# Kernel tuning notes

Measured on AMD Instinct MI355X. Metric: run time of the kernel, lower is better.

## Reference

```python
import jax, jax.numpy as jnp
import numpy as np

NQ = 4       # num_qubits
DEPTH = 2
NC = 4       # num_classes
DIM = 2 ** NQ
EPS = 1e-5   # BatchNorm1d eps


def _cz_diag():
    # diagonal of the CZ chain on wires (0,1),(1,2),(2,3); wire w -> bit (NQ-1-w)
    d = np.ones(DIM, np.float32)
    for i in range(NQ - 1):
        for k in range(DIM):
            if ((k >> (NQ - 1 - i)) & 1) and ((k >> (NQ - 2 - i)) & 1):
                d[k] *= -1.0
    return jnp.asarray(d.astype(np.complex64))


def _zmat():
    # ZMAT[k, w] = <k|Z_w|k>
    z = np.empty((DIM, NQ), np.float32)
    for k in range(DIM):
        for w in range(NQ):
            z[k, w] = 1.0 - 2.0 * ((k >> (NQ - 1 - w)) & 1)
    return jnp.asarray(z)


CZ_DIAG = _cz_diag()
ZMAT = _zmat()


def _apply_1q(state, gate, wire):
    # state: [B, DIM] complex64; gate: [2,2] (shared) or [B,2,2] (batched)
    B = state.shape[0]
    left, right = 2 ** wire, 2 ** (NQ - 1 - wire)
    s = state.reshape(B, left, 2, right)
    if gate.ndim == 2:
        s = jnp.einsum('ij,bljr->blir', gate, s)
    else:
        s = jnp.einsum('bij,bljr->blir', gate, s)
    return s.reshape(B, DIM)


def _circuit(pooled, weights):
    # pooled: [B, NQ] angles; weights: [DEPTH*NQ]
    B = pooled.shape[0]
    state = jnp.zeros((B, DIM), jnp.complex64).at[:, 0].set(1.0)
    # RX(pooled[:, i]) on wire i  (batched gates)
    for i in range(NQ):
        th = pooled[:, i] * 0.5
        c, s = jnp.cos(th), jnp.sin(th)
        g = jnp.stack([jnp.stack([c, -1j * s], -1),
                       jnp.stack([-1j * s, c], -1)], -2)  # [B,2,2] complex64
        state = _apply_1q(state, g, i)
    idx = 0
    for _ in range(DEPTH):
        # RY(weights[idx]) on each wire (real 2x2, shared across batch)
        for i in range(NQ):
            th = weights[idx] * 0.5
            idx += 1
            c, s = jnp.cos(th), jnp.sin(th)
            g = jnp.stack([jnp.stack([c, -s]), jnp.stack([s, c])])  # [2,2]
            state = _apply_1q(state, g, i)
        # CZ chain = diagonal sign flips
        state = state * CZ_DIAG
    probs = state.real ** 2 + state.imag ** 2          # [B, DIM]
    return probs @ ZMAT                                # [B, NQ] expvals of Z_w


def setup_inputs() -> dict:
    B = 262144
    keys = jax.random.split(jax.random.key(0), 4)
    x = jax.random.normal(keys[0], (B, 1, 12, 12), jnp.float32)
    weights = jax.random.normal(keys[1], (DEPTH * NQ,), jnp.float32)
    W = jax.random.normal(keys[2], (NC, NQ), jnp.float32) * 0.5
    b = jax.random.normal(keys[3], (NC,), jnp.float32) * 0.1
    gamma = jnp.ones((NC,), jnp.float32)
    beta = jnp.zeros((NC,), jnp.float32)
    return {'x': x, 'weights': weights, 'W': W, 'b': b,
            'gamma': gamma, 'beta': beta}


def reference(x, weights, W, b, gamma, beta):
    B = x.shape[0]
    # avg_pool2d(x, 6): [B,1,12,12] -> [B,1,2,2] -> [B,4]
    pooled = x.reshape(B, 1, 2, 6, 2, 6).mean(axis=(3, 5)).reshape(B, NQ)
    q = _circuit(pooled, weights)                      # [B, NQ]
    logits = q @ W.T + b                               # [B, NC]
    # BatchNorm1d, training mode: batch mean / biased variance
    mean = logits.mean(axis=0)
    var = logits.var(axis=0)
    return (logits - mean) / jnp.sqrt(var + EPS) * gamma + beta
```

## Files before the change

kernel.cpp:

```cpp
#include <hip/hip_runtime.h>
#include <hip/hip_bf16.h>


__device__ __forceinline__ float bfbits2f(unsigned short u) {
    return __uint_as_float(((unsigned int)u) << 16);
}
__device__ __forceinline__ float ldp(const void* p, int i, bool isbf16) {
    if (isbf16) return bfbits2f(((const unsigned short*)p)[i]);
    return ((const float*)p)[i];
}
__device__ __forceinline__ int quad_of(int e) {
    return ((e / 12) / 6) * 2 + ((e % 12) / 6);
}

__global__ __launch_bounds__(256) void qcircuit_kernel(
    const void* __restrict__ x,
    const void* __restrict__ wts,
    const void* __restrict__ Wm,
    const void* __restrict__ bias,
    const void* __restrict__ gamma,
    float* __restrict__ logits,
    float* __restrict__ partials,
    int B)
{
    const int b = blockIdx.x * blockDim.x + threadIdx.x;
    if (b >= B) return;

    const bool isbf16 = (*(const unsigned int*)gamma) == 0x3F803F80u;

    float sums[4] = {0.f, 0.f, 0.f, 0.f};
    if (isbf16) {
        const uint4* px = reinterpret_cast<const uint4*>(x) + (size_t)b * 18;
        uint4 v[18];
#pragma unroll
        for (int i = 0; i < 18; ++i) v[i] = px[i];
#pragma unroll
        for (int i = 0; i < 18; ++i) {
            unsigned int wrd[4] = {v[i].x, v[i].y, v[i].z, v[i].w};
#pragma unroll
            for (int c = 0; c < 4; ++c) {
                const int e0 = i * 8 + c * 2;
                sums[quad_of(e0)]     += __uint_as_float(wrd[c] << 16);
                sums[quad_of(e0 + 1)] += __uint_as_float(wrd[c] & 0xffff0000u);
            }
        }
    } else {
        const float4* px = reinterpret_cast<const float4*>(x) + (size_t)b * 36;
#pragma unroll
        for (int i = 0; i < 36; ++i) {
            float4 t = px[i];
            const int e0 = i * 4;
            sums[quad_of(e0)]     += t.x;
            sums[quad_of(e0 + 1)] += t.y;
            sums[quad_of(e0 + 2)] += t.z;
            sums[quad_of(e0 + 3)] += t.w;
        }
    }

    const float pscale = 0.5f / 36.0f;
    float cg[4], sg[4];
#pragma unroll
    for (int w = 0; w < 4; ++w) {
        float th = sums[w] * pscale;
        sincosf(th, &sg[w], &cg[w]);
    }

    float f[16];
#pragma unroll
    for (int k = 0; k < 16; ++k) {
        float a0 = (k & 8) ? sg[0] : cg[0];
        float a1 = (k & 4) ? sg[1] : cg[1];
        float a2 = (k & 2) ? sg[2] : cg[2];
        float a3 = (k & 1) ? sg[3] : cg[3];
        f[k] = (a0 * a1) * (a2 * a3);
    }
    float re[16], im[16];
#pragma unroll
    for (int k = 0; k < 16; ++k) {
        int pc = __popc(k) & 3;
        re[k] = (pc == 0) ? f[k] : ((pc == 2) ? -f[k] : 0.f);
        im[k] = (pc == 3) ? f[k] : ((pc == 1) ? -f[k] : 0.f);
    }

    float wc[8], wsn[8];
#pragma unroll
    for (int i = 0; i < 8; ++i) {
        float th = ldp(wts, i, isbf16) * 0.5f;
        sincosf(th, &wsn[i], &wc[i]);
    }

#pragma unroll
    for (int d = 0; d < 2; ++d) {
#pragma unroll
        for (int w = 0; w < 4; ++w) {
            const float cc = wc[d * 4 + w], ss = wsn[d * 4 + w];
            const int m = 1 << (3 - w);
#pragma unroll
            for (int k0 = 0; k0 < 16; ++k0) {
                if (k0 & m) continue;
                const int k1 = k0 | m;
                float r0 = re[k0], r1 = re[k1];
                re[k0] = cc * r0 - ss * r1;
                re[k1] = ss * r0 + cc * r1;
                float i0 = im[k0], i1 = im[k1];
                im[k0] = cc * i0 - ss * i1;
                im[k1] = ss * i0 + cc * i1;
            }
        }
#pragma unroll
        for (int k = 0; k < 16; ++k) {
            if ((0xB848u >> k) & 1u) { re[k] = -re[k]; im[k] = -im[k]; }
        }
    }

    float pr[16];
#pragma unroll
    for (int k = 0; k < 16; ++k) pr[k] = re[k] * re[k] + im[k] * im[k];
    float q[4];
#pragma unroll
    for (int w = 0; w < 4; ++w) {
        const int m = 1 << (3 - w);
        float acc = 0.f;
#pragma unroll
        for (int k = 0; k < 16; ++k) acc += (k & m) ? -pr[k] : pr[k];
        q[w] = acc;
    }

    float lg[4];
#pragma unroll
    for (int c = 0; c < 4; ++c) {
        float acc = ldp(bias, c, isbf16);
#pragma unroll
        for (int w = 0; w < 4; ++w) acc += q[w] * ldp(Wm, c * 4 + w, isbf16);
        lg[c] = acc;
    }
    reinterpret_cast<float4*>(logits)[b] = make_float4(lg[0], lg[1], lg[2], lg[3]);

    float rs[8];
#pragma unroll
    for (int c = 0; c < 4; ++c) { rs[c] = lg[c]; rs[4 + c] = lg[c] * lg[c]; }
#pragma unroll
    for (int off = 32; off > 0; off >>= 1) {
#pragma unroll
        for (int i = 0; i < 8; ++i) rs[i] += __shfl_down(rs[i], off, 64);
    }
    __shared__ float red[4][8];
    if ((threadIdx.x & 63) == 0) {
#pragma unroll
        for (int i = 0; i < 8; ++i) red[threadIdx.x >> 6][i] = rs[i];
    }
    __syncthreads();
    if (threadIdx.x < 8) {
        partials[(size_t)blockIdx.x * 8 + threadIdx.x] =
            red[0][threadIdx.x] + red[1][threadIdx.x] +
            red[2][threadIdx.x] + red[3][threadIdx.x];
    }
}

__global__ __launch_bounds__(256) void reduce_kernel(
    const float* __restrict__ partials, float* __restrict__ finals, int nblocks)
{
    float acc[8] = {0.f, 0.f, 0.f, 0.f, 0.f, 0.f, 0.f, 0.f};
    for (int r = threadIdx.x; r < nblocks; r += 256) {
#pragma unroll
        for (int i = 0; i < 8; ++i) acc[i] += partials[(size_t)r * 8 + i];
    }
#pragma unroll
    for (int off = 32; off > 0; off >>= 1) {
#pragma unroll
        for (int i = 0; i < 8; ++i) acc[i] += __shfl_down(acc[i], off, 64);
    }
    __shared__ float red[4][8];
    if ((threadIdx.x & 63) == 0) {
#pragma unroll
        for (int i = 0; i < 8; ++i) red[threadIdx.x >> 6][i] = acc[i];
    }
    __syncthreads();
    if (threadIdx.x < 8) {
        finals[threadIdx.x] = red[0][threadIdx.x] + red[1][threadIdx.x] +
                              red[2][threadIdx.x] + red[3][threadIdx.x];
    }
}

__global__ __launch_bounds__(256) void bn_kernel(
    const float* __restrict__ logits,
    const float* __restrict__ finals,
    const void* __restrict__ gamma,
    const void* __restrict__ beta,
    void* __restrict__ out,
    int B)
{
    const int b = blockIdx.x * blockDim.x + threadIdx.x;
    if (b >= B) return;
    const bool isbf16 = (*(const unsigned int*)gamma) == 0x3F803F80u;
    const float invB = 1.0f / (float)B;
    float4 l = reinterpret_cast<const float4*>(logits)[b];
    float lv[4] = {l.x, l.y, l.z, l.w};
    float ov[4];
#pragma unroll
    for (int c = 0; c < 4; ++c) {
        float mean = finals[c] * invB;
        float var  = finals[4 + c] * invB - mean * mean;
        float sc   = ldp(gamma, c, isbf16) * rsqrtf(var + 1e-5f);
        ov[c] = (lv[c] - mean) * sc + ldp(beta, c, isbf16);
    }
    if (isbf16) {
        unsigned short ub[4];
#pragma unroll
        for (int c = 0; c < 4; ++c) {
            __hip_bfloat16 h = __float2bfloat16(ov[c]);
            ub[c] = *reinterpret_cast<unsigned short*>(&h);
        }
        reinterpret_cast<ushort4*>(out)[b] = make_ushort4(ub[0], ub[1], ub[2], ub[3]);
    } else {
        reinterpret_cast<float4*>(out)[b] = make_float4(ov[0], ov[1], ov[2], ov[3]);
    }
}

extern "C" void kernel_launch(void* const* d_in, const int* in_sizes, int n_in,
                              void* d_out, int out_size, void* d_ws, size_t ws_size,
                              hipStream_t stream)
{
    const void* x     = d_in[0];
    const void* wts   = d_in[1];
    const void* Wm    = d_in[2];
    const void* bias  = d_in[3];
    const void* gamma = d_in[4];
    const void* beta  = d_in[5];

    const int B = in_sizes[0] / 144;
    const int nblocks = (B + 255) / 256;

    float* partials = (float*)d_ws;
    float* finals   = (float*)((char*)d_ws + 64 * 1024);
    float* logits   = (float*)((char*)d_ws + 128 * 1024);

    dim3 blk(256), grd(nblocks);
    qcircuit_kernel<<<grd, blk, 0, stream>>>(x, wts, Wm, bias, gamma,
                                             logits, partials, B);
    reduce_kernel<<<1, blk, 0, stream>>>(partials, finals, nblocks);
    bn_kernel<<<grd, blk, 0, stream>>>(logits, finals, gamma, beta, d_out, B);
}
```

Measured before the change: 232.9 us.

## Stage input tiles through LDS for coalesced loads before pooling

Rewrites the pooling stage so each block loads 64-sample tiles of x with coalesced thread-contiguous vector loads into padded shared memory. Four threads per sample then sum one 6x6 quadrant each from LDS. The aim is to replace the per-thread strided 576-byte reads, which coalesce poorly, with fully coalesced global traffic. In exchange it adds about 37KB of LDS, which may lower occupancy, adds several syncthreads, and drops the tail handling, so B must be a multiple of 256.

```diff
diff --git a/kernel.cpp b/kernel.cpp
--- a/kernel.cpp
+++ b/kernel.cpp
@@ -1,6 +1,8 @@
 #include <hip/hip_runtime.h>
 #include <hip/hip_bf16.h>
 
+
+#define PAD 145
 
 __device__ __forceinline__ float bfbits2f(unsigned short u) {
     return __uint_as_float(((unsigned int)u) << 16);
@@ -8,9 +10,6 @@
 __device__ __forceinline__ float ldp(const void* p, int i, bool isbf16) {
     if (isbf16) return bfbits2f(((const unsigned short*)p)[i]);
     return ((const float*)p)[i];
-}
-__device__ __forceinline__ int quad_of(int e) {
-    return ((e / 12) / 6) * 2 + ((e % 12) / 6);
 }
 
 __global__ __launch_bounds__(256) void qcircuit_kernel(
@@ -23,45 +22,67 @@
     float* __restrict__ partials,
     int B)
 {
-    const int b = blockIdx.x * blockDim.x + threadIdx.x;
-    if (b >= B) return;
-
+    const int t = threadIdx.x;
     const bool isbf16 = (*(const unsigned int*)gamma) == 0x3F803F80u;
 
-    float sums[4] = {0.f, 0.f, 0.f, 0.f};
-    if (isbf16) {
-        const uint4* px = reinterpret_cast<const uint4*>(x) + (size_t)b * 18;
-        uint4 v[18];
-#pragma unroll
-        for (int i = 0; i < 18; ++i) v[i] = px[i];
-#pragma unroll
-        for (int i = 0; i < 18; ++i) {
-            unsigned int wrd[4] = {v[i].x, v[i].y, v[i].z, v[i].w};
-#pragma unroll
-            for (int c = 0; c < 4; ++c) {
-                const int e0 = i * 8 + c * 2;
-                sums[quad_of(e0)]     += __uint_as_float(wrd[c] << 16);
-                sums[quad_of(e0 + 1)] += __uint_as_float(wrd[c] & 0xffff0000u);
+    __shared__ float lds_elem[64 * PAD];
+    __shared__ float lds_pool[256 * 5];
+    __shared__ float red[4][8];
+
+    const int s_b = t >> 2, q_b = t & 3;
+    const int r0 = (q_b >> 1) * 6, c0 = (q_b & 1) * 6;
+
+#pragma unroll
+    for (int T = 0; T < 4; ++T) {
+        const size_t sample0 = (size_t)blockIdx.x * 256 + T * 64;
+
+        if (isbf16) {
+            const uint2* src = reinterpret_cast<const uint2*>(x) + sample0 * 36;
+#pragma unroll
+            for (int k = 0; k < 9; ++k) {
+                const int f  = t + 256 * k;
+                uint2 v = src[f];
+                const int e4 = f * 4;
+                const int s  = e4 / 144;
+                const int e  = e4 - s * 144;
+                float* dst = &lds_elem[s * PAD + e];
+                dst[0] = __uint_as_float(v.x << 16);
+                dst[1] = __uint_as_float(v.x & 0xffff0000u);
+                dst[2] = __uint_as_float(v.y << 16);
+                dst[3] = __uint_as_float(v.y & 0xffff0000u);
             }
-        }
-    } else {
-        const float4* px = reinterpret_cast<const float4*>(x) + (size_t)b * 36;
-#pragma unroll
-        for (int i = 0; i < 36; ++i) {
-            float4 t = px[i];
-            const int e0 = i * 4;
-            sums[quad_of(e0)]     += t.x;
-            sums[quad_of(e0 + 1)] += t.y;
-            sums[quad_of(e0 + 2)] += t.z;
-            sums[quad_of(e0 + 3)] += t.w;
-        }
+        } else {
+            const float4* src = reinterpret_cast<const float4*>(x) + sample0 * 36;
+#pragma unroll
+            for (int k = 0; k < 9; ++k) {
+                const int f  = t + 256 * k;
+                float4 v = src[f];
+                const int e4 = f * 4;
+                const int s  = e4 / 144;
+                const int e  = e4 - s * 144;
+                float* dst = &lds_elem[s * PAD + e];
+                dst[0] = v.x; dst[1] = v.y; dst[2] = v.z; dst[3] = v.w;
+            }
+        }
+        __syncthreads();
+
+        {
+            float acc = 0.f;
+            const float* base = &lds_elem[s_b * PAD + r0 * 12 + c0];
+#pragma unroll
+            for (int r = 0; r < 6; ++r)
+#pragma unroll
+                for (int c = 0; c < 6; ++c) acc += base[r * 12 + c];
+            lds_pool[(T * 64 + s_b) * 5 + q_b] = acc;
+        }
+        __syncthreads();
     }
 
     const float pscale = 0.5f / 36.0f;
     float cg[4], sg[4];
 #pragma unroll
     for (int w = 0; w < 4; ++w) {
-        float th = sums[w] * pscale;
+        float th = lds_pool[t * 5 + w] * pscale;
         sincosf(th, &sg[w], &cg[w]);
     }
 
@@ -99,9 +120,9 @@
             for (int k0 = 0; k0 < 16; ++k0) {
                 if (k0 & m) continue;
                 const int k1 = k0 | m;
-                float r0 = re[k0], r1 = re[k1];
-                re[k0] = cc * r0 - ss * r1;
-                re[k1] = ss * r0 + cc * r1;
+                float rr0 = re[k0], rr1 = re[k1];
+                re[k0] = cc * rr0 - ss * rr1;
+                re[k1] = ss * rr0 + cc * rr1;
                 float i0 = im[k0], i1 = im[k1];
                 im[k0] = cc * i0 - ss * i1;
                 im[k1] = ss * i0 + cc * i1;
@@ -134,6 +155,7 @@
         for (int w = 0; w < 4; ++w) acc += q[w] * ldp(Wm, c * 4 + w, isbf16);
         lg[c] = acc;
     }
+    const size_t b = (size_t)blockIdx.x * 256 + t;
     reinterpret_cast<float4*>(logits)[b] = make_float4(lg[0], lg[1], lg[2], lg[3]);
 
     float rs[8];
@@ -144,16 +166,14 @@
 #pragma unroll
         for (int i = 0; i < 8; ++i) rs[i] += __shfl_down(rs[i], off, 64);
     }
-    __shared__ float red[4][8];
-    if ((threadIdx.x & 63) == 0) {
-#pragma unroll
-        for (int i = 0; i < 8; ++i) red[threadIdx.x >> 6][i] = rs[i];
+    if ((t & 63) == 0) {
+#pragma unroll
+        for (int i = 0; i < 8; ++i) red[t >> 6][i] = rs[i];
     }
     __syncthreads();
-    if (threadIdx.x < 8) {
-        partials[(size_t)blockIdx.x * 8 + threadIdx.x] =
-            red[0][threadIdx.x] + red[1][threadIdx.x] +
-            red[2][threadIdx.x] + red[3][threadIdx.x];
+    if (t < 8) {
+        partials[(size_t)blockIdx.x * 8 + t] =
+            red[0][t] + red[1][t] + red[2][t] + red[3][t];
     }
 }
 
@@ -229,15 +249,16 @@
     const void* beta  = d_in[5];
 
     const int B = in_sizes[0] / 144;
-    const int nblocks = (B + 255) / 256;
+    const int nblocks = B / 256;
 
     float* partials = (float*)d_ws;
     float* finals   = (float*)((char*)d_ws + 64 * 1024);
     float* logits   = (float*)((char*)d_ws + 128 * 1024);
 
-    dim3 blk(256), grd(nblocks);
-    qcircuit_kernel<<<grd, blk, 0, stream>>>(x, wts, Wm, bias, gamma,
-                                             logits, partials, B);
-    reduce_kernel<<<1, blk, 0, stream>>>(partials, finals, nblocks);
-    bn_kernel<<<grd, blk, 0, stream>>>(logits, finals, gamma, beta, d_out, B);
-}
+    dim3 blk(256);
+    qcircuit_kernel<<<dim3(nblocks), blk, 0, stream>>>(x, wts, Wm, bias, gamma,
+                                                       logits, partials, B);
+    reduce_kernel<<<dim3(1), blk, 0, stream>>>(partials, finals, nblocks);
+    bn_kernel<<<dim3((B + 255) / 256), blk, 0, stream>>>(logits, finals, gamma, beta,
+                                                         d_out, B);
+}
```

Result: no change. 232.6 us (-0.1%).
